# Kernel tuning notes

Hardware: AMD Instinct MI355X
Metric: run time of the kernel (lower is better)

## Reference

```python
import jax, jax.numpy as jnp
import numpy as np

P_ITER = 30   # Krylov iterations (p_iter=30 in source)
N_PROBE = 100 # stochastic probe vectors (t=100 in source)


def setup_inputs() -> dict:
    N, t, r = 8192, N_PROBE, 256
    key = jax.random.key(0)
    kA, ky, kz = jax.random.split(key, 3)
    # Well-conditioned SPD kernel + noise matrix: K = A A^T / r + I
    A = jax.random.normal(kA, (N, r), dtype=jnp.float32)
    Knn_noise = (A @ A.T) / r + jnp.eye(N, dtype=jnp.float32)
    y = jax.random.normal(ky, (N, 1), dtype=jnp.float32)
    # Rademacher probes (||z||^2 = N exactly)
    Z = jnp.where(jax.random.normal(kz, (N, t)) >= 0, 1.0, -1.0).astype(jnp.float32)
    return {"Knn_noise": Knn_noise, "y": y, "Z": Z}


def _batched_cg(K, B, p_iter):
    """Batched conjugate gradients on K X = B, tracking Lanczos coefficients.
    B: [N, M]. Returns X [N, M], alphas [p, M], betas [p, M]."""
    X = jnp.zeros_like(B)
    R = B
    P = B
    rs = jnp.sum(R * R, axis=0)  # [M]

    def step(carry, _):
        X, R, P, rs = carry
        V = K @ P                               # [N, M] dense matvec (GEMM)
        pv = jnp.sum(P * V, axis=0)             # [M]
        alpha = rs / pv
        X = X + alpha * P
        R = R - alpha * V
        rs_new = jnp.sum(R * R, axis=0)
        beta = rs_new / rs
        P = R + beta * P
        return (X, R, P, rs_new), (alpha, beta)

    (X, _, _, _), (alphas, betas) = jax.lax.scan(step, (X, R, P, rs), None, length=p_iter)
    return X, alphas, betas


def _slq_logdet(alphas, betas, N):
    """Stochastic Lanczos quadrature logdet from CG coefficients.
    alphas, betas: [p, t] (one column per probe)."""
    inv_a = 1.0 / alphas                                   # [p, t]
    diag = inv_a.at[1:].add(betas[:-1] / alphas[:-1])      # T diagonal  [p, t]
    off = jnp.sqrt(betas[:-1]) / alphas[:-1]               # T off-diag  [p-1, t]

    def make_T(d, o):
        return jnp.diag(d) + jnp.diag(o, 1) + jnp.diag(o, -1)

    Ts = jax.vmap(make_T, in_axes=(1, 1))(diag, off)       # [t, p, p]
    lam, V = jnp.linalg.eigh(Ts)                           # small p x p eig per probe
    lam = jnp.maximum(lam, 1e-12)
    # z^T log(K) z ~= ||z||^2 * e1^T Vexp log(Lam) V^T e1 ; ||z||^2 = N (Rademacher)
    quad = jnp.sum(V[:, 0, :] ** 2 * jnp.log(lam), axis=1)  # [t]
    return N * jnp.mean(quad)


def reference(Knn_noise, y, Z):
    N = y.shape[0]
    B = jnp.concatenate([y, Z], axis=1)                    # solve + probes together
    X, alphas, betas = _batched_cg(Knn_noise, B, P_ITER)
    Knn_i_y = X[:, :1]                                     # K^{-1} y
    log_det = _slq_logdet(alphas[:, 1:], betas[:, 1:], N)  # SLQ logdet from probes
    two_pi = jnp.asarray(2.0 * np.pi, dtype=y.dtype)
    return -0.5 * (y.T @ Knn_i_y) - 0.5 * log_det - N * 0.5 * jnp.log(two_pi)
```

## Files before the change

kernel.cpp:

```cpp
#include <hip/hip_runtime.h>
#include <hip/hip_bf16.h>

#define NN 8192
#define NCOLS 101
#define CPW 112
#define CPAD 128
#define BM 64
#define KSPL 4
#define KCH (NN / KSPL)
#define NSTEP (KCH / 128)
#define PITER 30
#define PVLD 104

typedef __attribute__((ext_vector_type(4))) float f32x4;

__device__ __forceinline__ void async_copy16(const void* g, void* l) {
  __builtin_amdgcn_global_load_lds(
      (const __attribute__((address_space(1))) unsigned int*)g,
      (__attribute__((address_space(3))) unsigned int*)l, 16, 0, 0);
}

__device__ __forceinline__ unsigned int pack_fp8x4(float x, float y, float z, float w) {
  unsigned int v = __builtin_amdgcn_cvt_pk_fp8_f32(x, y, 0, false);
  v = __builtin_amdgcn_cvt_pk_fp8_f32(z, w, v, true);
  return v;
}

__device__ __forceinline__ float block_sum(float v) {
  #pragma unroll
  for (int o = 32; o > 0; o >>= 1) v += __shfl_down(v, o);
  __shared__ float sw[4];
  int w = threadIdx.x >> 6;
  if ((threadIdx.x & 63) == 0) sw[w] = v;
  __syncthreads();
  float r = 0.f;
  if (threadIdx.x < 4) r = sw[threadIdx.x];
  r += __shfl_down(r, 2);
  r += __shfl_down(r, 1);
  return r;
}

__global__ __launch_bounds__(256, 2) void gemm_kernel(
    const unsigned char* __restrict__ Kb,
    const unsigned char* __restrict__ Pb,
    const float* __restrict__ Pf,
    const float* __restrict__ SCit,
    float* __restrict__ Vp,
    float* __restrict__ pvp) {
  __shared__ __align__(16) unsigned char smem[49152];
  unsigned char* sA = smem;
  unsigned char* sB = smem + 16384;
  float* sC = (float*)smem;

  int bx = blockIdx.x;
  int rb = bx & 127;
  int kz = bx >> 7;
  int tid = threadIdx.x;
  int lane = tid & 63;
  int w = tid >> 6;
  int r0 = rb * BM;
  int k0 = kz * KCH;
  int lrow = lane >> 3;
  int gseg = (lane & 7) ^ lrow;
  int mm = lane & 15;
  int quad = lane >> 4;

  f32x4 acc[7];
  #pragma unroll
  for (int i = 0; i < 7; ++i) acc[i] = (f32x4){0.f, 0.f, 0.f, 0.f};

  auto stage = [&](int s, int buf) {
    int kk = k0 + s * 128;
    #pragma unroll
    for (int q = 0; q < 2; ++q) {
      async_copy16(Kb + (size_t)(r0 + w * 16 + q * 8 + lrow) * NN + kk + gseg * 16,
                   sA + buf * 8192 + (w * 16 + q * 8) * 128);
    }
    #pragma unroll
    for (int q = 0; q < 4; ++q) {
      async_copy16(Pb + (size_t)(w * 32 + q * 8 + lrow) * NN + kk + gseg * 16,
                   sB + buf * 16384 + (w * 32 + q * 8) * 128);
    }
  };

  stage(0, 0);
  __syncthreads();

  int arow = w * 16 + mm;
  #pragma unroll 2
  for (int s = 0; s < NSTEP; ++s) {
    int cur = s & 1;
    if (s + 1 < NSTEP) stage(s + 1, cur ^ 1);
    const unsigned char* A = sA + cur * 8192;
    const unsigned char* B = sB + cur * 16384;
    #pragma unroll
    for (int kh = 0; kh < 4; ++kh) {
      int seg16 = kh * 2 + (quad >> 1);
      long long aF = *(const long long*)(A + arow * 128 +
                     ((seg16 ^ (arow & 7)) << 4) + ((quad & 1) << 3));
      #pragma unroll
      for (int ct = 0; ct < 7; ++ct) {
        int bcol = ct * 16 + mm;
        long long bF = *(const long long*)(B + bcol * 128 +
                       ((seg16 ^ (bcol & 7)) << 4) + ((quad & 1) << 3));
        acc[ct] = __builtin_amdgcn_mfma_f32_16x16x32_fp8_fp8(aF, bF, acc[ct], 0, 0, 0);
      }
    }
    __syncthreads();
  }
  #pragma unroll
  for (int ct = 0; ct < 7; ++ct)
    #pragma unroll
    for (int r = 0; r < 4; ++r)
      sC[(w * 16 + quad * 4 + r) * 113 + ct * 16 + mm] = acc[ct][r];
  __syncthreads();
  float* Vout = Vp + (size_t)kz * ((size_t)CPW * NN);
  for (int idx = tid; idx < BM * CPW; idx += 256) {
    int col = idx >> 6;
    int row = idx & 63;
    if (col < NCOLS)
      Vout[(size_t)col * NN + r0 + row] = sC[row * 113 + col] * SCit[col];
  }
  int rr = tid & 63;
  int g = tid >> 6;
  for (int j = 0; j < 28; ++j) {
    int c = g + j * 4;
    float prod = 0.f;
    if (c < NCOLS)
      prod = sC[rr * 113 + c] * SCit[c] * Pf[(size_t)c * NN + r0 + rr];
    #pragma unroll
    for (int o = 32; o > 0; o >>= 1) prod += __shfl_down(prod, o);
    if (rr == 0 && c < NCOLS) pvp[(size_t)bx * PVLD + c] = prod;
  }
}

__global__ void update1_kernel(const float* __restrict__ Vp,
                               const float* __restrict__ Pf,
                               float* __restrict__ R,
                               float* __restrict__ X0,
                               const float* __restrict__ pvp,
                               const float* __restrict__ rs,
                               float* __restrict__ rs_new,
                               float* __restrict__ alphas) {
  const size_t SPL = (size_t)CPW * NN;
  __shared__ float s_alpha;
  int c = blockIdx.y;
  int t = threadIdx.x;
  float pvv = pvp[(size_t)t * PVLD + c] + pvp[(size_t)(t + 256) * PVLD + c];
  float pvtot = block_sum(pvv);
  if (t == 0) s_alpha = rs[c] / pvtot;
  __syncthreads();
  float alpha = s_alpha;

  size_t off = (size_t)c * NN + blockIdx.x * 1024 + t * 4;
  float4 a = *(const float4*)(Vp + off);
  float4 b = *(const float4*)(Vp + SPL + off);
  float4 d = *(const float4*)(Vp + 2 * SPL + off);
  float4 e = *(const float4*)(Vp + 3 * SPL + off);
  float4 v;
  v.x = a.x + b.x + d.x + e.x;
  v.y = a.y + b.y + d.y + e.y;
  v.z = a.z + b.z + d.z + e.z;
  v.w = a.w + b.w + d.w + e.w;
  float4 r = *(float4*)(R + off);
  r.x -= alpha * v.x; r.y -= alpha * v.y; r.z -= alpha * v.z; r.w -= alpha * v.w;
  *(float4*)(R + off) = r;
  if (c == 0) {
    size_t xo = blockIdx.x * 1024 + t * 4;
    float4 x = *(float4*)(X0 + xo);
    float4 p = *(const float4*)(Pf + off);
    x.x += alpha * p.x; x.y += alpha * p.y; x.z += alpha * p.z; x.w += alpha * p.w;
    *(float4*)(X0 + xo) = x;
  }
  float rn = r.x * r.x + r.y * r.y + r.z * r.z + r.w * r.w;
  float tot = block_sum(rn);
  if (t == 0) {
    atomicAdd(rs_new + c, tot);
    if (blockIdx.x == 0) alphas[c] = alpha;
  }
}

__global__ void update2_kernel(const float* __restrict__ R,
                               float* __restrict__ P,
                               unsigned char* __restrict__ Pb,
                               const float* __restrict__ rs,
                               const float* __restrict__ rs_new,
                               const float* __restrict__ PNold,
                               float* __restrict__ PNnew,
                               float* __restrict__ SCnew,
                               float* __restrict__ betas) {
  int c = blockIdx.y;
  float rsn = rs_new[c];
  float beta = rsn / rs[c];
  float pnn = rsn + beta * beta * PNold[c];
  float sc = exp2f(roundf(0.5f * log2f(pnn * (1.f / 8192.f))));
  float inv = 1.f / sc;
  size_t off = (size_t)c * NN + blockIdx.x * 1024 + threadIdx.x * 4;
  float4 r = *(const float4*)(R + off);
  float4 p = *(float4*)(P + off);
  p.x = r.x + beta * p.x; p.y = r.y + beta * p.y;
  p.z = r.z + beta * p.z; p.w = r.w + beta * p.w;
  *(float4*)(P + off) = p;
  *(unsigned int*)(Pb + off) = pack_fp8x4(p.x * inv, p.y * inv, p.z * inv, p.w * inv);
  if (threadIdx.x == 0 && blockIdx.x == 0) {
    betas[c] = beta;
    PNnew[c] = pnn;
    SCnew[c] = sc;
  }
}

__global__ void cast_k_kernel(const float* __restrict__ K, unsigned char* __restrict__ Kb) {
  size_t i = ((size_t)blockIdx.x * 256 + threadIdx.x) * 4;
  size_t stride = (size_t)gridDim.x * 1024;
  for (; i < (size_t)NN * NN; i += stride) {
    float4 f = *(const float4*)(K + i);
    *(unsigned int*)(Kb + i) = pack_fp8x4(f.x, f.y, f.z, f.w);
  }
}

__global__ void init_vec_kernel(const float* __restrict__ y, const float* __restrict__ Z,
                                float* __restrict__ P, float* __restrict__ R,
                                unsigned char* __restrict__ Pb) {
  int c = blockIdx.y;
  int i = blockIdx.x * 256 + threadIdx.x;
  float val = (c == 0) ? y[i] : Z[(size_t)i * 100 + (c - 1)];
  size_t off = (size_t)c * NN + i;
  P[off] = val;
  R[off] = val;
  Pb[off] = (unsigned char)(__builtin_amdgcn_cvt_pk_fp8_f32(val, 0.f, 0, false) & 0xFF);
}

#define NSMALL 23424
__global__ void init_misc_kernel(float* __restrict__ X0, float* __restrict__ smalls,
                                 unsigned char* __restrict__ Pbpad) {
  const int total = 8192 + NSMALL + 27 * NN;
  for (int t = blockIdx.x * 256 + threadIdx.x; t < total; t += gridDim.x * 256) {
    if (t < 8192) X0[t] = 0.f;
    else if (t < 8192 + NSMALL) smalls[t - 8192] = 0.f;
    else Pbpad[t - (8192 + NSMALL)] = 0;
  }
}

__global__ void init_rs_kernel(const float* __restrict__ y, float* __restrict__ rs0,
                               float* __restrict__ pn0, float* __restrict__ sc0) {
  int t = threadIdx.x;
  float s = 0.f;
  for (int i = t; i < NN; i += 256) { float v = y[i]; s += v * v; }
  float tot = block_sum(s);
  if (t == 0) { rs0[0] = tot; pn0[0] = tot; }
  if (t >= 1 && t <= 100) { rs0[t] = (float)NN; pn0[t] = (float)NN; }
  if (t < 128) sc0[t] = 1.f;
}

__global__ __launch_bounds__(64, 1) void slq_kernel(
    const float* __restrict__ AL, const float* __restrict__ BE,
    float* __restrict__ QP) {
  __shared__ double sd[PITER], se[PITER];
  int lane = threadIdx.x;
  int c = blockIdx.x + 1;
  if (lane < PITER) {
    double a = (double)AL[lane * 128 + c];
    double dd = 1.0 / a;
    if (lane > 0) {
      double ap = (double)AL[(lane - 1) * 128 + c];
      double bp = (double)BE[(lane - 1) * 128 + c];
      dd += bp / ap;
    }
    sd[lane] = dd;
    double ee = 0.0;
    if (lane < PITER - 1) {
      double b = (double)BE[lane * 128 + c];
      ee = sqrt(b) / a;
    }
    se[lane] = ee;
  }
  __syncthreads();
  double d[PITER], e[PITER];
  #pragma unroll
  for (int i = 0; i < PITER; ++i) { d[i] = sd[i]; e[i] = se[i]; }

  float quadk = 0.f;
  if (lane < PITER) {
    double lo = 1e300, hi = -1e300;
    #pragma unroll
    for (int i = 0; i < PITER; ++i) {
      double r = e[i] + (i > 0 ? e[i - 1] : 0.0);
      lo = fmin(lo, d[i] - r);
      hi = fmax(hi, d[i] + r);
    }
    int k = lane;
    for (int it = 0; it < 48; ++it) {
      double mid = 0.5 * (lo + hi);
      int cnt = 0;
      double q = d[0] - mid;
      cnt += (q < 0.0);
      #pragma unroll
      for (int i = 1; i < PITER; ++i) {
        double aq = fabs(q);
        if (aq < 1e-30) q = (q < 0.0) ? -1e-30 : 1e-30;
        q = d[i] - mid - (e[i - 1] * e[i - 1]) / q;
        cnt += (q < 0.0);
      }
      if (cnt > k) hi = mid; else lo = mid;
    }
    double lam = 0.5 * (lo + hi);
    double e0 = fmax(e[0], 1e-150);
    double vprev = 1.0;
    double vcur = (lam - d[0]) / e0;
    double s = 1.0 + vcur * vcur;
    double scale2 = 1.0;
    #pragma unroll
    for (int i = 1; i < PITER - 1; ++i) {
      double ei = fmax(e[i], 1e-150);
      double vnext = ((lam - d[i]) * vcur - e[i - 1] * vprev) / ei;
      if (fabs(vnext) > 1e150) {
        vnext *= 1e-150; vcur *= 1e-150; s *= 1e-300; scale2 *= 1e-300;
      }
      vprev = vcur; vcur = vnext;
      s += vcur * vcur;
    }
    double w = scale2 / s;
    double lc = lam > 1e-12 ? lam : 1e-12;
    quadk = (float)(w * log(lc));
  }
  #pragma unroll
  for (int o = 32; o > 0; o >>= 1) quadk += __shfl_down(quadk, o);
  if (lane == 0) QP[blockIdx.x] = quadk;
}

__global__ void final2_kernel(const float* __restrict__ y, const float* __restrict__ X0,
                              const float* __restrict__ QP, float* __restrict__ out) {
  int t = threadIdx.x;
  float s = 0.f;
  for (int i = t; i < NN; i += 256) s += y[i] * X0[i];
  float ydot = block_sum(s);
  __syncthreads();
  float q = (t < 100) ? QP[t] : 0.f;
  float qsum = block_sum(q);
  if (t == 0) {
    float logdet = (float)NN * (qsum * 0.01f);
    out[0] = -0.5f * ydot - 0.5f * logdet - (float)NN * 0.5f * 1.8378770664093454f;
  }
}

extern "C" void kernel_launch(void* const* d_in, const int* in_sizes, int n_in,
                              void* d_out, int out_size, void* d_ws, size_t ws_size,
                              hipStream_t stream) {
  const float* K = (const float*)d_in[0];
  const float* y = (const float*)d_in[1];
  const float* Z = (const float*)d_in[2];
  float* out = (float*)d_out;
  char* ws = (char*)d_ws;
  if (ws_size < 89796096ull) return;

  unsigned char* Kb = (unsigned char*)(ws + 0ull);
  unsigned char* Pb = (unsigned char*)(ws + 67108864ull);
  float* P   = (float*)(ws + 68157440ull);
  float* R   = (float*)(ws + 71467008ull);
  float* Vp  = (float*)(ws + 74776576ull);
  float* X0  = (float*)(ws + 89456640ull);
  float* PVP = (float*)(ws + 89489408ull);
  float* SM  = (float*)(ws + 89702400ull);
  float* RS = SM;
  float* AL = SM + 7808;
  float* BE = SM + 11648;
  float* PN = SM + 15488;
  float* SC = SM + 19456;
  float* QP = Vp;

  cast_k_kernel<<<8192, 256, 0, stream>>>(K, Kb);
  init_vec_kernel<<<dim3(32, 101), 256, 0, stream>>>(y, Z, P, R, Pb);
  init_misc_kernel<<<240, 256, 0, stream>>>(X0, SM, Pb + (size_t)NCOLS * NN);
  init_rs_kernel<<<1, 256, 0, stream>>>(y, RS, PN, SC);

  for (int it = 0; it < PITER; ++it) {
    gemm_kernel<<<512, 256, 0, stream>>>(Kb, Pb, P, SC + it * 128, Vp, PVP);
    update1_kernel<<<dim3(8, 101), 256, 0, stream>>>(Vp, P, R, X0, PVP,
        RS + it * 128, RS + (it + 1) * 128, AL + it * 128);
    update2_kernel<<<dim3(8, 101), 256, 0, stream>>>(R, P, Pb, RS + it * 128,
        RS + (it + 1) * 128, PN + it * 128, PN + (it + 1) * 128,
        SC + (it + 1) * 128, BE + it * 128);
  }
  slq_kernel<<<100, 64, 0, stream>>>(AL, BE, QP);
  final2_kernel<<<1, 256, 0, stream>>>(y, X0, QP, out);
}
```

Measured before the change: 1.901 ms.

## Use 128x128 GEMM tiles with 8-way K split and fp16 partials

Retiles the fp8 MFMA GEMM from 64-row tiles with 7 column tiles per wave into 128x128 block tiles, where each wave computes a 64x64 4x4 MFMA grid. This gives more operand reuse per LDS load. The K split goes from 4 to 8 so the grid stays at 512 blocks. The split-K partial V results are now stored as fp16 instead of fp32, which keeps partial-sum traffic roughly constant despite twice as many splits but adds rounding error in the CG residual update. LDS use grows to 64KB and the block computes padding columns up to 128, which is wasted MFMA work.

```diff
diff --git a/kernel.cpp b/kernel.cpp
--- a/kernel.cpp
+++ b/kernel.cpp
@@ -1,12 +1,12 @@
 #include <hip/hip_runtime.h>
-#include <hip/hip_bf16.h>
+#include <hip/hip_fp16.h>
 
 #define NN 8192
 #define NCOLS 101
 #define CPW 112
-#define CPAD 128
-#define BM 64
-#define KSPL 4
+#define BN 128
+#define BM 128
+#define KSPL 8
 #define KCH (NN / KSPL)
 #define NSTEP (KCH / 128)
 #define PITER 30
@@ -45,16 +45,16 @@
     const unsigned char* __restrict__ Pb,
     const float* __restrict__ Pf,
     const float* __restrict__ SCit,
-    float* __restrict__ Vp,
+    __half* __restrict__ Vp,
     float* __restrict__ pvp) {
-  __shared__ __align__(16) unsigned char smem[49152];
+  __shared__ __align__(16) unsigned char smem[65536];
   unsigned char* sA = smem;
-  unsigned char* sB = smem + 16384;
+  unsigned char* sB = smem + 32768;
   float* sC = (float*)smem;
 
   int bx = blockIdx.x;
-  int rb = bx & 127;
-  int kz = bx >> 7;
+  int kz = bx & 7;
+  int rb = bx >> 3;
   int tid = threadIdx.x;
   int lane = tid & 63;
   int w = tid >> 6;
@@ -64,20 +64,32 @@
   int gseg = (lane & 7) ^ lrow;
   int mm = lane & 15;
   int quad = lane >> 4;
-
-  f32x4 acc[7];
-  #pragma unroll
-  for (int i = 0; i < 7; ++i) acc[i] = (f32x4){0.f, 0.f, 0.f, 0.f};
+  int q1 = quad >> 1, q0 = quad & 1;
+  int wm = w >> 1, wn = w & 1;
+
+  int aBase[4], aXor[4], bBase[4], bXor[4];
+  #pragma unroll
+  for (int i = 0; i < 4; ++i) {
+    int arow = wm * 64 + i * 16 + mm;
+    aBase[i] = arow * 128 + (q0 << 3);
+    aXor[i] = (arow & 7) << 4;
+    int bcol = wn * 64 + i * 16 + mm;
+    bBase[i] = bcol * 128 + (q0 << 3);
+    bXor[i] = (bcol & 7) << 4;
+  }
+
+  f32x4 acc[4][4];
+  #pragma unroll
+  for (int i = 0; i < 4; ++i)
+    #pragma unroll
+    for (int j = 0; j < 4; ++j) acc[i][j] = (f32x4){0.f, 0.f, 0.f, 0.f};
 
   auto stage = [&](int s, int buf) {
     int kk = k0 + s * 128;
     #pragma unroll
-    for (int q = 0; q < 2; ++q) {
-      async_copy16(Kb + (size_t)(r0 + w * 16 + q * 8 + lrow) * NN + kk + gseg * 16,
-                   sA + buf * 8192 + (w * 16 + q * 8) * 128);
-    }
-    #pragma unroll
     for (int q = 0; q < 4; ++q) {
+      async_copy16(Kb + (size_t)(r0 + w * 32 + q * 8 + lrow) * NN + kk + gseg * 16,
+                   sA + buf * 16384 + (w * 32 + q * 8) * 128);
       async_copy16(Pb + (size_t)(w * 32 + q * 8 + lrow) * NN + kk + gseg * 16,
                    sB + buf * 16384 + (w * 32 + q * 8) * 128);
     }
@@ -86,55 +98,63 @@
   stage(0, 0);
   __syncthreads();
 
-  int arow = w * 16 + mm;
   #pragma unroll 2
   for (int s = 0; s < NSTEP; ++s) {
     int cur = s & 1;
     if (s + 1 < NSTEP) stage(s + 1, cur ^ 1);
-    const unsigned char* A = sA + cur * 8192;
+    const unsigned char* A = sA + cur * 16384;
     const unsigned char* B = sB + cur * 16384;
     #pragma unroll
     for (int kh = 0; kh < 4; ++kh) {
-      int seg16 = kh * 2 + (quad >> 1);
-      long long aF = *(const long long*)(A + arow * 128 +
-                     ((seg16 ^ (arow & 7)) << 4) + ((quad & 1) << 3));
+      int s16 = (kh * 2 + q1) << 4;
+      long long aF[4], bF[4];
       #pragma unroll
-      for (int ct = 0; ct < 7; ++ct) {
-        int bcol = ct * 16 + mm;
-        long long bF = *(const long long*)(B + bcol * 128 +
-                       ((seg16 ^ (bcol & 7)) << 4) + ((quad & 1) << 3));
-        acc[ct] = __builtin_amdgcn_mfma_f32_16x16x32_fp8_fp8(aF, bF, acc[ct], 0, 0, 0);
+      for (int i = 0; i < 4; ++i) {
+        aF[i] = *(const long long*)(A + aBase[i] + (s16 ^ aXor[i]));
+        bF[i] = *(const long long*)(B + bBase[i] + (s16 ^ bXor[i]));
       }
+      #pragma unroll
+      for (int i = 0; i < 4; ++i)
+        #pragma unroll
+        for (int j = 0; j < 4; ++j)
+          acc[i][j] = __builtin_amdgcn_mfma_f32_16x16x32_fp8_fp8(aF[i], bF[j], acc[i][j], 0, 0, 0);
     }
     __syncthreads();
   }
   #pragma unroll
-  for (int ct = 0; ct < 7; ++ct)
-    #pragma unroll
-    for (int r = 0; r < 4; ++r)
-      sC[(w * 16 + quad * 4 + r) * 113 + ct * 16 + mm] = acc[ct][r];
-  __syncthreads();
-  float* Vout = Vp + (size_t)kz * ((size_t)CPW * NN);
+  for (int i = 0; i < 4; ++i)
+    #pragma unroll
+    for (int j = 0; j < 4; ++j) {
+      int ctile = wn * 64 + j * 16;
+      if (ctile >= CPW) continue;
+      #pragma unroll
+      for (int r = 0; r < 4; ++r)
+        sC[(wm * 64 + i * 16 + quad * 4 + r) * 113 + ctile + mm] = acc[i][j][r];
+    }
+  __syncthreads();
+  const size_t SPL = (size_t)CPW * NN;
+  __half* Vout = Vp + (size_t)kz * SPL;
   for (int idx = tid; idx < BM * CPW; idx += 256) {
-    int col = idx >> 6;
-    int row = idx & 63;
+    int col = idx >> 7;
+    int row = idx & 127;
     if (col < NCOLS)
-      Vout[(size_t)col * NN + r0 + row] = sC[row * 113 + col] * SCit[col];
+      Vout[(size_t)col * NN + r0 + row] = __float2half(sC[row * 113 + col] * SCit[col]);
   }
   int rr = tid & 63;
   int g = tid >> 6;
-  for (int j = 0; j < 28; ++j) {
+  for (int j = 0; j < 26; ++j) {
     int c = g + j * 4;
     float prod = 0.f;
     if (c < NCOLS)
-      prod = sC[rr * 113 + c] * SCit[c] * Pf[(size_t)c * NN + r0 + rr];
+      prod = (sC[rr * 113 + c] * Pf[(size_t)c * NN + r0 + rr] +
+              sC[(rr + 64) * 113 + c] * Pf[(size_t)c * NN + r0 + 64 + rr]) * SCit[c];
     #pragma unroll
     for (int o = 32; o > 0; o >>= 1) prod += __shfl_down(prod, o);
     if (rr == 0 && c < NCOLS) pvp[(size_t)bx * PVLD + c] = prod;
   }
 }
 
-__global__ void update1_kernel(const float* __restrict__ Vp,
+__global__ void update1_kernel(const __half* __restrict__ Vp,
                                const float* __restrict__ Pf,
                                float* __restrict__ R,
                                float* __restrict__ X0,
@@ -153,15 +173,14 @@
   float alpha = s_alpha;
 
   size_t off = (size_t)c * NN + blockIdx.x * 1024 + t * 4;
-  float4 a = *(const float4*)(Vp + off);
-  float4 b = *(const float4*)(Vp + SPL + off);
-  float4 d = *(const float4*)(Vp + 2 * SPL + off);
-  float4 e = *(const float4*)(Vp + 3 * SPL + off);
-  float4 v;
-  v.x = a.x + b.x + d.x + e.x;
-  v.y = a.y + b.y + d.y + e.y;
-  v.z = a.z + b.z + d.z + e.z;
-  v.w = a.w + b.w + d.w + e.w;
+  float4 v = {0.f, 0.f, 0.f, 0.f};
+  #pragma unroll
+  for (int sp = 0; sp < KSPL; ++sp) {
+    const __half2* p = (const __half2*)(Vp + sp * SPL + off);
+    float2 f01 = __half22float2(p[0]);
+    float2 f23 = __half22float2(p[1]);
+    v.x += f01.x; v.y += f01.y; v.z += f23.x; v.w += f23.y;
+  }
   float4 r = *(float4*)(R + off);
   r.x -= alpha * v.x; r.y -= alpha * v.y; r.z -= alpha * v.z; r.w -= alpha * v.w;
   *(float4*)(R + off) = r;
@@ -357,7 +376,7 @@
   unsigned char* Pb = (unsigned char*)(ws + 67108864ull);
   float* P   = (float*)(ws + 68157440ull);
   float* R   = (float*)(ws + 71467008ull);
-  float* Vp  = (float*)(ws + 74776576ull);
+  __half* Vp = (__half*)(ws + 74776576ull);
   float* X0  = (float*)(ws + 89456640ull);
   float* PVP = (float*)(ws + 89489408ull);
   float* SM  = (float*)(ws + 89702400ull);
@@ -366,7 +385,7 @@
   float* BE = SM + 11648;
   float* PN = SM + 15488;
   float* SC = SM + 19456;
-  float* QP = Vp;
+  float* QP = (float*)(ws + 74776576ull);
 
   cast_k_kernel<<<8192, 256, 0, stream>>>(K, Kb);
   init_vec_kernel<<<dim3(32, 101), 256, 0, stream>>>(y, Z, P, R, Pb);
```

Result: slower. 1.989 ms (+4.6%).
